# Kernel tuning notes

Measured on AMD Instinct MI355X. Metric: run time of the kernel, lower is better.

The kernel has to match this reference:

```python
import jax, jax.numpy as jnp
import numpy as np

EMBED_DIM = 1024
NUM_HEADS = 16
HEAD_DIM = EMBED_DIM // NUM_HEADS


def setup_inputs() -> dict:
    key = jax.random.key(0)
    k_x, k_wqkv, k_bqkv, k_wo, k_bo = jax.random.split(key, 5)
    b, n = 2, 2048
    scale_in = 1.0 / np.sqrt(EMBED_DIM)
    return {
        "x": jax.random.normal(k_x, (b, n, EMBED_DIM), dtype=jnp.float32),
        "W_qkv": jax.random.normal(k_wqkv, (EMBED_DIM, 3 * EMBED_DIM), dtype=jnp.float32) * scale_in,
        "b_qkv": jnp.zeros((3 * EMBED_DIM,), dtype=jnp.float32),
        "W_out": jax.random.normal(k_wo, (EMBED_DIM, EMBED_DIM), dtype=jnp.float32) * scale_in,
        "b_out": jnp.zeros((EMBED_DIM,), dtype=jnp.float32),
    }


def _rope_rotate(t, cos, sin):
    # t: [b, h, n, hd]; cos/sin: [1, 1, n, hd//2]
    t1, t2 = jnp.split(t, 2, axis=-1)
    return jnp.concatenate([cos * t1 - sin * t2, sin * t1 + cos * t2], axis=-1)


def reference(x, W_qkv, b_qkv, W_out, b_out):
    b, n, d = x.shape
    h, hd = NUM_HEADS, HEAD_DIM

    qkv = x @ W_qkv + b_qkv                      # [b, n, 3d]
    q, k, v = jnp.split(qkv, 3, axis=-1)
    q, k, v = [t.reshape(b, n, h, hd).transpose(0, 2, 1, 3) for t in (q, k, v)]

    # RoPE tables
    hd2 = hd // 2
    theta = 10000.0 ** (-2.0 * jnp.arange(hd2, dtype=jnp.float32) / hd)
    freqs = jnp.arange(n, dtype=jnp.float32)[:, None] * theta[None, :]  # [n, hd2]
    cos = jnp.cos(freqs)[None, None]
    sin = jnp.sin(freqs)[None, None]
    q = _rope_rotate(q, cos, sin)
    k = _rope_rotate(k, cos, sin)

    scores = jnp.einsum('bhqd,bhkd->bhqk', q, k) / jnp.sqrt(jnp.float32(hd))
    attn = jax.nn.softmax(scores, axis=-1)       # [b, h, n, n]
    out = jnp.einsum('bhqk,bhkd->bhqd', attn, v)
    out = out.transpose(0, 2, 1, 3).reshape(b, n, d)
    return out @ W_out + b_out
```

## Files before the change

kernel.cpp:

```cpp
#include <hip/hip_runtime.h>
#include <hip/hip_bf16.h>
#include <math.h>

#define EMBED 1024
#define NHEAD 16
#define HD 64
#define BATCH 2
#define SEQ 2048
#define MTOT (BATCH * SEQ)
#define QKVN (3 * EMBED)

typedef __attribute__((ext_vector_type(8))) short short8;
typedef __attribute__((ext_vector_type(4))) float f32x4;

typedef __attribute__((address_space(1))) const unsigned int GUI;
typedef __attribute__((address_space(3))) unsigned int LUI;

__device__ __forceinline__ void gload_lds16(const void* src, void* dst) {
  __builtin_amdgcn_global_load_lds((GUI*)src, (LUI*)dst, 16, 0, 0);
}

__device__ __forceinline__ unsigned short f2bf(float f) {
  unsigned u = __builtin_bit_cast(unsigned, f);
  u += 0x7fffu + ((u >> 16) & 1u);
  return (unsigned short)(u >> 16);
}

__device__ __forceinline__ unsigned cvt_pk_bf16(float lo, float hi) {
  unsigned r;
  asm("v_cvt_pk_bf16_f32 %0, %1, %2" : "=v"(r) : "v"(lo), "v"(hi));
  return r;
}

#define QSCALE 0.1803368801111191f


__global__ __launch_bounds__(256) void k_cvt(const float* __restrict__ in,
                                             unsigned short* __restrict__ out, int n4) {
  int i = blockIdx.x * 256 + threadIdx.x;
  if (i >= n4) return;
  float4 v = reinterpret_cast<const float4*>(in)[i];
  ushort4 o;
  o.x = f2bf(v.x); o.y = f2bf(v.y); o.z = f2bf(v.z); o.w = f2bf(v.w);
  reinterpret_cast<ushort4*>(out)[i] = o;
}

__global__ __launch_bounds__(256) void k_transpose_cvt(const float* __restrict__ W,
                                                       unsigned short* __restrict__ WT,
                                                       int K, int Ncols) {
  __shared__ float tile[32][33];
  int n0 = blockIdx.x * 32, k0 = blockIdx.y * 32;
  int tc = threadIdx.x & 31, tr = threadIdx.x >> 5;
  for (int i = 0; i < 4; i++) {
    int r = tr + i * 8;
    tile[r][tc] = W[(size_t)(k0 + r) * Ncols + n0 + tc];
  }
  __syncthreads();
  for (int i = 0; i < 4; i++) {
    int r = tr + i * 8;
    WT[(size_t)(n0 + r) * K + k0 + tc] = f2bf(tile[tc][r]);
  }
}

__global__ __launch_bounds__(256) void k_rope_tables(float* __restrict__ cosT,
                                                     float* __restrict__ sinT) {
  int idx = blockIdx.x * 256 + threadIdx.x;
  if (idx >= SEQ * 32) return;
  int pos = idx >> 5, i = idx & 31;
  float theta = __expf((float)i * -0.28782313662425575f);
  float f = (float)pos * theta;
  cosT[idx] = cosf(f);
  sinT[idx] = sinf(f);
}

__device__ __forceinline__ void gemm_mainloop(const unsigned short* __restrict__ A,
                                              const unsigned short* __restrict__ Bt,
                                              unsigned short* Al, unsigned short* Bl,
                                              size_t m0, size_t n0,
                                              int tid, int l15, int g, int wm, int wn,
                                              f32x4 acc[4][4]) {
  const int w = tid >> 6;
  const int lane = tid & 63;
  const int srow = lane >> 3, slot = lane & 7;
  for (int k0 = 0; k0 < 1024; k0 += 64) {
    __syncthreads();
    for (int it = 0; it < 4; it++) {
      const int r = w * 32 + it * 8 + srow;
      const int sc = (slot ^ (r & 7)) * 8;
      gload_lds16(A + (m0 + r) * 1024 + k0 + sc, &Al[(w * 32 + it * 8) * 64]);
      gload_lds16(Bt + (n0 + r) * 1024 + k0 + sc, &Bl[(w * 32 + it * 8) * 64]);
    }
    __syncthreads();
    for (int kk = 0; kk < 2; kk++) {
      short8 fa[4], fb[4];
      const int xr = ((kk * 4 + g) ^ (l15 & 7)) * 8;
      for (int i = 0; i < 4; i++)
        fa[i] = *reinterpret_cast<const short8*>(&Al[(wm * 64 + i * 16 + l15) * 64 + xr]);
      for (int j = 0; j < 4; j++)
        fb[j] = *reinterpret_cast<const short8*>(&Bl[(wn * 64 + j * 16 + l15) * 64 + xr]);
      for (int i = 0; i < 4; i++)
        for (int j = 0; j < 4; j++)
          acc[i][j] = __builtin_amdgcn_mfma_f32_16x16x32_bf16(fa[i], fb[j], acc[i][j], 0, 0, 0);
    }
  }
}

__global__ __launch_bounds__(256) void k_qkv_gemm(const unsigned short* __restrict__ A,
                                                  const unsigned short* __restrict__ Bt,
                                                  const float* __restrict__ bias,
                                                  const float* __restrict__ cosT,
                                                  const float* __restrict__ sinT,
                                                  unsigned short* __restrict__ Qb,
                                                  unsigned short* __restrict__ Kb,
                                                  unsigned short* __restrict__ Vtg) {
  __shared__ alignas(16) unsigned short Al[128 * 64];
  __shared__ alignas(16) unsigned short Bl[128 * 64];
  const int tid = threadIdx.x;
  const int lane = tid & 63, l15 = lane & 15, g = lane >> 4;
  const int wid = tid >> 6, wm = wid >> 1, wn = wid & 1;
  const size_t m0 = (size_t)blockIdx.y * 128;
  const size_t n0 = (size_t)blockIdx.x * 128;
  f32x4 acc[4][4] = {};
  gemm_mainloop(A, Bt, Al, Bl, m0, n0, tid, l15, g, wm, wn, acc);

  const int cbase = (int)n0 + wn * 64;
  const int sec = cbase >> 10;
  const int head = (cbase & 1023) >> 6;
  float bia[4];
  for (int j = 0; j < 4; j++) bia[j] = bias[cbase + j * 16 + l15];
  const size_t mw = m0 + wm * 64;

  if (sec == 2) {
    for (int i = 0; i < 4; i++) {
      size_t mbase = mw + i * 16 + g * 4;
      int bb = (int)(mbase >> 11), pos0 = (int)(mbase & 2047);
      int k0 = pos0 & 63;
      int col = (pos0 & ~63) | (k0 & 32) | (((k0 >> 2) & 3) << 3) | (((k0 >> 4) & 1) << 2);
      size_t hb = (size_t)(bb * NHEAD + head) * HD;
      for (int j = 0; j < 4; j++) {
        int d = j * 16 + l15;
        uint2 pk;
        pk.x = cvt_pk_bf16(acc[i][j][0] + bia[j], acc[i][j][1] + bia[j]);
        pk.y = cvt_pk_bf16(acc[i][j][2] + bia[j], acc[i][j][3] + bia[j]);
        *reinterpret_cast<uint2*>(Vtg + (hb + d) * SEQ + col) = pk;
      }
    }
  } else {
    unsigned short* dst = sec ? Kb : Qb;
    const float qs = sec ? 1.0f : QSCALE;
    for (int i = 0; i < 4; i++)
      for (int r = 0; r < 4; r++) {
        size_t m = mw + i * 16 + g * 4 + r;
        int bb = (int)(m >> 11), pos = (int)(m & 2047);
        size_t base = ((size_t)(bb * NHEAD + head) * SEQ + pos) * HD;
        const float* cr = cosT + pos * 32;
        const float* sr = sinT + pos * 32;
        for (int pl = 0; pl < 2; pl++) {
          int ii = pl * 16 + l15;
          float c = cr[ii], s = sr[ii];
          float lo = acc[i][pl][r] + bia[pl];
          float hi = acc[i][pl + 2][r] + bia[pl + 2];
          dst[base + ii]      = f2bf((c * lo - s * hi) * qs);
          dst[base + 32 + ii] = f2bf((s * lo + c * hi) * qs);
        }
      }
  }
}

__global__ __launch_bounds__(256) void k_out_gemm(const unsigned short* __restrict__ A,
                                                  const unsigned short* __restrict__ Bt,
                                                  const float* __restrict__ bias,
                                                  float* __restrict__ out) {
  __shared__ alignas(16) unsigned short Al[128 * 64];
  __shared__ alignas(16) unsigned short Bl[64 * 64];
  const int tid = threadIdx.x;
  const int lane = tid & 63, l15 = lane & 15, g = lane >> 4;
  const int wid = tid >> 6, wm = wid >> 1, wn = wid & 1;
  const int w = wid;
  const int srow = lane >> 3, slot = lane & 7;
  const size_t m0 = (size_t)blockIdx.y * 128;
  const size_t n0 = (size_t)blockIdx.x * 64;
  f32x4 acc[4][2] = {};

  for (int k0 = 0; k0 < 1024; k0 += 64) {
    __syncthreads();
    for (int it = 0; it < 4; it++) {
      const int r = w * 32 + it * 8 + srow;
      const int sc = (slot ^ (r & 7)) * 8;
      gload_lds16(A + (m0 + r) * 1024 + k0 + sc, &Al[(w * 32 + it * 8) * 64]);
    }
    for (int it = 0; it < 2; it++) {
      const int r = w * 16 + it * 8 + srow;
      const int sc = (slot ^ (r & 7)) * 8;
      gload_lds16(Bt + (n0 + r) * 1024 + k0 + sc, &Bl[(w * 16 + it * 8) * 64]);
    }
    __syncthreads();
    for (int kk = 0; kk < 2; kk++) {
      short8 fa[4], fb[2];
      const int xr = ((kk * 4 + g) ^ (l15 & 7)) * 8;
      for (int i = 0; i < 4; i++)
        fa[i] = *reinterpret_cast<const short8*>(&Al[(wm * 64 + i * 16 + l15) * 64 + xr]);
      for (int j = 0; j < 2; j++)
        fb[j] = *reinterpret_cast<const short8*>(&Bl[(wn * 32 + j * 16 + l15) * 64 + xr]);
      for (int i = 0; i < 4; i++)
        for (int j = 0; j < 2; j++)
          acc[i][j] = __builtin_amdgcn_mfma_f32_16x16x32_bf16(fa[i], fb[j], acc[i][j], 0, 0, 0);
    }
  }

  const int cbase = (int)n0 + wn * 32;
  const size_t mw = m0 + wm * 64;
  for (int i = 0; i < 4; i++)
    for (int r = 0; r < 4; r++) {
      size_t m = mw + i * 16 + g * 4 + r;
      for (int j = 0; j < 2; j++) {
        int col = cbase + j * 16 + l15;
        out[m * EMBED + col] = acc[i][j][r] + bias[col];
      }
    }
}

__global__ __launch_bounds__(256) void k_attn(const unsigned short* __restrict__ Q,
                                              const unsigned short* __restrict__ Kg,
                                              const unsigned short* __restrict__ Vtg,
                                              float* __restrict__ Opart,
                                              float* __restrict__ lpart) {
  __shared__ alignas(16) unsigned short Kt[2][64 * 64];
  __shared__ alignas(16) unsigned short Vt[2][64 * 64];
  const int tid = threadIdx.x, w = tid >> 6, lane = tid & 63;
  const int l15 = lane & 15, g = lane >> 4;
  const int srow = lane >> 3, slot = lane & 7;

  const int n = blockIdx.x;
  const int xcd = n & 7, m = n >> 3;
  const int qb = m & 15, z = m >> 4;
  const int sp = z & 1, bh = (z >> 1) * 8 + xcd;

  const unsigned short* Qp = Q + (size_t)bh * SEQ * HD;
  const unsigned short* Kp = Kg + (size_t)bh * SEQ * HD;
  const unsigned short* Vp = Vtg + (size_t)bh * HD * SEQ;
  const int q0 = qb * 128 + w * 32;

  short8 aq[2][2];
#pragma unroll
  for (int u = 0; u < 2; u++)
#pragma unroll
    for (int kk = 0; kk < 2; kk++)
      aq[u][kk] = *reinterpret_cast<const short8*>(
          Qp + (size_t)(q0 + u * 16 + l15) * HD + kk * 32 + g * 8);

  const int sr16 = w * 16 + srow;
  const int sc0 = (slot ^ (sr16 & 7)) * 8;
  const int kb0 = sp * 1024;

  f32x4 o[2][4] = {};
  float lrow[2] = {0.f, 0.f};

#define STAGE(tt, b)                                                             \
  do {                                                                           \
    const int kb_ = kb0 + (tt) * 64;                                             \
    gload_lds16(Kp + (size_t)(kb_ + sr16) * HD + sc0, &Kt[b][(w * 16) * 64]);    \
    gload_lds16(Vp + (size_t)sr16 * SEQ + kb_ + sc0, &Vt[b][(w * 16) * 64]);     \
    gload_lds16(Kp + (size_t)(kb_ + sr16 + 8) * HD + sc0,                        \
                &Kt[b][(w * 16 + 8) * 64]);                                      \
    gload_lds16(Vp + (size_t)(sr16 + 8) * SEQ + kb_ + sc0,                       \
                &Vt[b][(w * 16 + 8) * 64]);                                      \
  } while (0)

#define COMPUTE(cur)                                                             \
  do {                                                                           \
    const unsigned short* Ktc = Kt[cur];                                         \
    const unsigned short* Vtc = Vt[cur];                                         \
    f32x4 s[2][4] = {};                                                          \
    _Pragma("unroll") for (int kk = 0; kk < 2; kk++) {                           \
      const int xr = ((kk * 4 + g) ^ (l15 & 7)) * 8;                             \
      _Pragma("unroll") for (int c = 0; c < 4; c++) {                            \
        short8 ak = *reinterpret_cast<const short8*>(&Ktc[(c * 16 + l15) * 64 + xr]); \
        s[0][c] = __builtin_amdgcn_mfma_f32_16x16x32_bf16(ak, aq[0][kk], s[0][c], 0, 0, 0); \
        s[1][c] = __builtin_amdgcn_mfma_f32_16x16x32_bf16(ak, aq[1][kk], s[1][c], 0, 0, 0); \
      }                                                                          \
    }                                                                            \
    unsigned wpk[2][8];                                                          \
    _Pragma("unroll") for (int u = 0; u < 2; u++) {                              \
      float rs = 0.f;                                                            \
      _Pragma("unroll") for (int c = 0; c < 4; c++) {                            \
        float p0 = __builtin_exp2f(s[u][c][0]);                                  \
        float p1 = __builtin_exp2f(s[u][c][1]);                                  \
        float p2 = __builtin_exp2f(s[u][c][2]);                                  \
        float p3 = __builtin_exp2f(s[u][c][3]);                                  \
        rs += (p0 + p1) + (p2 + p3);                                             \
        wpk[u][2 * c]     = cvt_pk_bf16(p0, p1);                                 \
        wpk[u][2 * c + 1] = cvt_pk_bf16(p2, p3);                                 \
      }                                                                          \
      lrow[u] += rs;                                                             \
    }                                                                            \
    _Pragma("unroll") for (int kk = 0; kk < 2; kk++) {                           \
      const int xr = ((kk * 4 + g) ^ (l15 & 7)) * 8;                             \
      short8 pb0 = __builtin_bit_cast(short8,                                    \
          uint4{wpk[0][4 * kk], wpk[0][4 * kk + 1], wpk[0][4 * kk + 2], wpk[0][4 * kk + 3]}); \
      short8 pb1 = __builtin_bit_cast(short8,                                    \
          uint4{wpk[1][4 * kk], wpk[1][4 * kk + 1], wpk[1][4 * kk + 2], wpk[1][4 * kk + 3]}); \
      _Pragma("unroll") for (int c2 = 0; c2 < 4; c2++) {                         \
        short8 av = *reinterpret_cast<const short8*>(&Vtc[(c2 * 16 + l15) * 64 + xr]); \
        o[0][c2] = __builtin_amdgcn_mfma_f32_16x16x32_bf16(av, pb0, o[0][c2], 0, 0, 0); \
        o[1][c2] = __builtin_amdgcn_mfma_f32_16x16x32_bf16(av, pb1, o[1][c2], 0, 0, 0); \
      }                                                                          \
    }                                                                            \
  } while (0)

  STAGE(0, 0);

  for (int t = 0; t < 15; t++) {
    const int cur = t & 1;
    STAGE(t + 1, cur ^ 1);
    asm volatile("s_waitcnt vmcnt(4)" ::: "memory");
    __builtin_amdgcn_s_barrier();
    COMPUTE(cur);
    __builtin_amdgcn_s_barrier();
  }
  asm volatile("s_waitcnt vmcnt(0)" ::: "memory");
  __builtin_amdgcn_s_barrier();
  COMPUTE(1);

#undef STAGE
#undef COMPUTE

  const size_t ob = (size_t)(sp * 32 + bh) * HD * SEQ;
#pragma unroll
  for (int u = 0; u < 2; u++) {
    float l = lrow[u];
    l += __shfl_xor(l, 16, 64);
    l += __shfl_xor(l, 32, 64);
    const int pos = q0 + u * 16 + l15;
    if (g == 0) lpart[(size_t)(sp * 32 + bh) * SEQ + pos] = l;
#pragma unroll
    for (int c2 = 0; c2 < 4; c2++)
#pragma unroll
      for (int r = 0; r < 4; r++)
        Opart[ob + (size_t)(c2 * 16 + g * 4 + r) * SEQ + pos] = o[u][c2][r];
  }
}

__global__ __launch_bounds__(256) void k_merge(const float* __restrict__ Op,
                                               const float* __restrict__ lp,
                                               unsigned short* __restrict__ AO) {
  __shared__ float T[64][65];
  __shared__ float Ls[64];
  const int tid = threadIdx.x;
  const int bh = blockIdx.x & 31, pt = blockIdx.x >> 5;
  const int p0 = pt * 64;
  const size_t b0 = (size_t)bh * HD * SEQ;
  const size_t b1 = (size_t)(32 + bh) * HD * SEQ;
  const int pc = tid & 63, dr = tid >> 6;
#pragma unroll
  for (int pass = 0; pass < 16; pass++) {
    const int d = pass * 4 + dr;
    T[d][pc] = Op[b0 + (size_t)d * SEQ + p0 + pc] + Op[b1 + (size_t)d * SEQ + p0 + pc];
  }
  if (tid < 64)
    Ls[tid] = lp[(size_t)bh * SEQ + p0 + tid] + lp[(size_t)(32 + bh) * SEQ + p0 + tid];
  __syncthreads();
  const int pos = tid >> 2, dc = (tid & 3) * 16;
  const float inv = 1.f / Ls[pos];
  const int bb = bh >> 4, h = bh & 15;
  unsigned short* dst = AO + ((size_t)bb * SEQ + p0 + pos) * EMBED + h * HD + dc;
  unsigned pk[8];
#pragma unroll
  for (int i = 0; i < 8; i++)
    pk[i] = cvt_pk_bf16(T[dc + 2 * i][pos] * inv, T[dc + 2 * i + 1][pos] * inv);
  *reinterpret_cast<uint4*>(dst) = uint4{pk[0], pk[1], pk[2], pk[3]};
  *reinterpret_cast<uint4*>(dst + 8) = uint4{pk[4], pk[5], pk[6], pk[7]};
}

extern "C" void kernel_launch(void* const* d_in, const int* in_sizes, int n_in,
                              void* d_out, int out_size, void* d_ws, size_t ws_size,
                              hipStream_t stream) {
  const float* x    = (const float*)d_in[0];
  const float* Wqkv = (const float*)d_in[1];
  const float* bqkv = (const float*)d_in[2];
  const float* Wout = (const float*)d_in[3];
  const float* bout = (const float*)d_in[4];
  float* out = (float*)d_out;

  char* ws = (char*)d_ws;
  size_t off = 0;
  auto carve = [&](size_t bytes) {
    char* p = ws + off;
    off += (bytes + 255) & ~(size_t)255;
    return p;
  };
  float* cosT           = (float*)carve((size_t)SEQ * 32 * 4);
  float* sinT           = (float*)carve((size_t)SEQ * 32 * 4);
  unsigned short* Xb    = (unsigned short*)carve((size_t)MTOT * EMBED * 2);
  unsigned short* WqkvT = (unsigned short*)carve((size_t)QKVN * EMBED * 2);
  unsigned short* WoT   = (unsigned short*)carve((size_t)EMBED * EMBED * 2);
  unsigned short* Qb    = (unsigned short*)carve((size_t)MTOT * EMBED * 2);
  unsigned short* Kb    = (unsigned short*)carve((size_t)MTOT * EMBED * 2);
  unsigned short* Vtg   = (unsigned short*)carve((size_t)MTOT * EMBED * 2);
  unsigned short* AO    = (unsigned short*)carve((size_t)MTOT * EMBED * 2);
  float* Opart          = (float*)carve((size_t)2 * 32 * HD * SEQ * 4);
  float* lpart          = (float*)carve((size_t)2 * 32 * SEQ * 4);

  k_cvt<<<(MTOT * EMBED / 4 + 255) / 256, 256, 0, stream>>>(x, Xb, MTOT * EMBED / 4);
  k_transpose_cvt<<<dim3(QKVN / 32, EMBED / 32), 256, 0, stream>>>(Wqkv, WqkvT, EMBED, QKVN);
  k_transpose_cvt<<<dim3(EMBED / 32, EMBED / 32), 256, 0, stream>>>(Wout, WoT, EMBED, EMBED);
  k_rope_tables<<<(SEQ * 32) / 256, 256, 0, stream>>>(cosT, sinT);

  k_qkv_gemm<<<dim3(QKVN / 128, MTOT / 128), 256, 0, stream>>>(Xb, WqkvT, bqkv, cosT, sinT, Qb, Kb, Vtg);
  k_attn<<<dim3(1024), 256, 0, stream>>>(Qb, Kb, Vtg, Opart, lpart);
  k_merge<<<dim3(1024), 256, 0, stream>>>(Opart, lpart, AO);
  k_out_gemm<<<dim3(EMBED / 64, MTOT / 128), 256, 0, stream>>>(AO, WoT, bout, out);
}
```

Baseline: 146.7 us.

## Store attention partials row-major and simplify merge; use native exp2 and zero-init MFMA

Result: faster. 139.1 us (-5.1%).

```diff
diff --git a/kernel.cpp b/kernel.cpp
--- a/kernel.cpp
+++ b/kernel.cpp
@@ -31,6 +31,12 @@
   asm("v_cvt_pk_bf16_f32 %0, %1, %2" : "=v"(r) : "v"(lo), "v"(hi));
   return r;
 }
+
+#if __has_builtin(__builtin_amdgcn_exp2f)
+#define EXP2(x) __builtin_amdgcn_exp2f(x)
+#else
+#define EXP2(x) __builtin_exp2f(x)
+#endif
 
 #define QSCALE 0.1803368801111191f
 
@@ -253,6 +259,7 @@
   const int sc0 = (slot ^ (sr16 & 7)) * 8;
   const int kb0 = sp * 1024;
 
+  const f32x4 z4 = {0.f, 0.f, 0.f, 0.f};
   f32x4 o[2][4] = {};
   float lrow[2] = {0.f, 0.f};
 
@@ -271,23 +278,31 @@
   do {                                                                           \
     const unsigned short* Ktc = Kt[cur];                                         \
     const unsigned short* Vtc = Vt[cur];                                         \
-    f32x4 s[2][4] = {};                                                          \
-    _Pragma("unroll") for (int kk = 0; kk < 2; kk++) {                           \
-      const int xr = ((kk * 4 + g) ^ (l15 & 7)) * 8;                             \
+    f32x4 s[2][4];                                                               \
+    {                                                                            \
+      const int xr = (g ^ (l15 & 7)) * 8;                                        \
       _Pragma("unroll") for (int c = 0; c < 4; c++) {                            \
         short8 ak = *reinterpret_cast<const short8*>(&Ktc[(c * 16 + l15) * 64 + xr]); \
-        s[0][c] = __builtin_amdgcn_mfma_f32_16x16x32_bf16(ak, aq[0][kk], s[0][c], 0, 0, 0); \
-        s[1][c] = __builtin_amdgcn_mfma_f32_16x16x32_bf16(ak, aq[1][kk], s[1][c], 0, 0, 0); \
+        s[0][c] = __builtin_amdgcn_mfma_f32_16x16x32_bf16(ak, aq[0][0], z4, 0, 0, 0); \
+        s[1][c] = __builtin_amdgcn_mfma_f32_16x16x32_bf16(ak, aq[1][0], z4, 0, 0, 0); \
+      }                                                                          \
+    }                                                                            \
+    {                                                                            \
+      const int xr = ((4 + g) ^ (l15 & 7)) * 8;                                  \
+      _Pragma("unroll") for (int c = 0; c < 4; c++) {                            \
+        short8 ak = *reinterpret_cast<const short8*>(&Ktc[(c * 16 + l15) * 64 + xr]); \
+        s[0][c] = __builtin_amdgcn_mfma_f32_16x16x32_bf16(ak, aq[0][1], s[0][c], 0, 0, 0); \
+        s[1][c] = __builtin_amdgcn_mfma_f32_16x16x32_bf16(ak, aq[1][1], s[1][c], 0, 0, 0); \
       }                                                                          \
     }                                                                            \
     unsigned wpk[2][8];                                                          \
     _Pragma("unroll") for (int u = 0; u < 2; u++) {                              \
       float rs = 0.f;                                                            \
       _Pragma("unroll") for (int c = 0; c < 4; c++) {                            \
-        float p0 = __builtin_exp2f(s[u][c][0]);                                  \
-        float p1 = __builtin_exp2f(s[u][c][1]);                                  \
-        float p2 = __builtin_exp2f(s[u][c][2]);                                  \
-        float p3 = __builtin_exp2f(s[u][c][3]);                                  \
+        float p0 = EXP2(s[u][c][0]);                                             \
+        float p1 = EXP2(s[u][c][1]);                                             \
+        float p2 = EXP2(s[u][c][2]);                                             \
+        float p3 = EXP2(s[u][c][3]);                                             \
         rs += (p0 + p1) + (p2 + p3);                                             \
         wpk[u][2 * c]     = cvt_pk_bf16(p0, p1);                                 \
         wpk[u][2 * c + 1] = cvt_pk_bf16(p2, p3);                                 \
@@ -325,7 +340,7 @@
 #undef STAGE
 #undef COMPUTE
 
-  const size_t ob = (size_t)(sp * 32 + bh) * HD * SEQ;
+  const size_t ob = (size_t)(sp * 32 + bh) * SEQ * HD;
 #pragma unroll
   for (int u = 0; u < 2; u++) {
     float l = lrow[u];
@@ -333,42 +348,34 @@
     l += __shfl_xor(l, 32, 64);
     const int pos = q0 + u * 16 + l15;
     if (g == 0) lpart[(size_t)(sp * 32 + bh) * SEQ + pos] = l;
+    float* orow = Opart + ob + (size_t)pos * HD;
 #pragma unroll
     for (int c2 = 0; c2 < 4; c2++)
-#pragma unroll
-      for (int r = 0; r < 4; r++)
-        Opart[ob + (size_t)(c2 * 16 + g * 4 + r) * SEQ + pos] = o[u][c2][r];
+      *reinterpret_cast<f32x4*>(orow + c2 * 16 + g * 4) = o[u][c2];
   }
 }
 
 __global__ __launch_bounds__(256) void k_merge(const float* __restrict__ Op,
                                                const float* __restrict__ lp,
                                                unsigned short* __restrict__ AO) {
-  __shared__ float T[64][65];
-  __shared__ float Ls[64];
-  const int tid = threadIdx.x;
-  const int bh = blockIdx.x & 31, pt = blockIdx.x >> 5;
-  const int p0 = pt * 64;
-  const size_t b0 = (size_t)bh * HD * SEQ;
-  const size_t b1 = (size_t)(32 + bh) * HD * SEQ;
-  const int pc = tid & 63, dr = tid >> 6;
-#pragma unroll
-  for (int pass = 0; pass < 16; pass++) {
-    const int d = pass * 4 + dr;
-    T[d][pc] = Op[b0 + (size_t)d * SEQ + p0 + pc] + Op[b1 + (size_t)d * SEQ + p0 + pc];
-  }
-  if (tid < 64)
-    Ls[tid] = lp[(size_t)bh * SEQ + p0 + tid] + lp[(size_t)(32 + bh) * SEQ + p0 + tid];
-  __syncthreads();
-  const int pos = tid >> 2, dc = (tid & 3) * 16;
-  const float inv = 1.f / Ls[pos];
-  const int bb = bh >> 4, h = bh & 15;
-  unsigned short* dst = AO + ((size_t)bb * SEQ + p0 + pos) * EMBED + h * HD + dc;
+  const int t = threadIdx.x;
+  const int bh = blockIdx.x >> 5, pt = blockIdx.x & 31;
+  const int pos = pt * 64 + (t >> 2), dc = (t & 3) * 16;
+  const float* p0 = Op + ((size_t)bh * SEQ + pos) * HD + dc;
+  const float* p1 = p0 + (size_t)32 * SEQ * HD;
+  const float l = lp[(size_t)bh * SEQ + pos] + lp[(size_t)(32 + bh) * SEQ + pos];
+  const float inv = 1.f / l;
   unsigned pk[8];
 #pragma unroll
-  for (int i = 0; i < 8; i++)
-    pk[i] = cvt_pk_bf16(T[dc + 2 * i][pos] * inv, T[dc + 2 * i + 1][pos] * inv);
-  *reinterpret_cast<uint4*>(dst) = uint4{pk[0], pk[1], pk[2], pk[3]};
+  for (int i = 0; i < 4; i++) {
+    float4 a = reinterpret_cast<const float4*>(p0)[i];
+    float4 b = reinterpret_cast<const float4*>(p1)[i];
+    pk[2 * i]     = cvt_pk_bf16((a.x + b.x) * inv, (a.y + b.y) * inv);
+    pk[2 * i + 1] = cvt_pk_bf16((a.z + b.z) * inv, (a.w + b.w) * inv);
+  }
+  const int bb = bh >> 4, h = bh & 15;
+  unsigned short* dst = AO + ((size_t)bb * SEQ + pos) * EMBED + h * HD + dc;
+  *reinterpret_cast<uint4*>(dst)     = uint4{pk[0], pk[1], pk[2], pk[3]};
   *reinterpret_cast<uint4*>(dst + 8) = uint4{pk[4], pk[5], pk[6], pk[7]};
 }
 
```
